# Optimization experiments

Measured on AMD Instinct MI355X. Metric: run time of the kernel, lower is better.

## Reference

```python
import jax, jax.numpy as jnp
import numpy as np

N = 100000      # nodes
E = 800000      # directed edges per branch
HID = 128
FOUT = 128
HEADS = 2
LAYERS = 3      # convlayer
JK_LAYERS = 3
H2 = (JK_LAYERS * HID) // 2   # PyG JK-LSTM hidden size = 192
N_AA = 26
N_SS = 3


def setup_inputs() -> dict:
    key = jax.random.key(0)
    ks = iter(jax.random.split(key, 32))
    def nrm(shape, scale=0.05):
        return jax.random.normal(next(ks), shape, dtype=jnp.float32) * scale
    return {
        "x_idx": jax.random.randint(next(ks), (N, 2), 0, N_SS),
        "x_flt": jax.random.normal(next(ks), (N, 5), dtype=jnp.float32),
        "edge_index_l": jax.random.randint(next(ks), (2, E), 0, N),
        "edge_index_r": jax.random.randint(next(ks), (2, E), 0, N),
        "emb_aa": nrm((2, N_AA, HID - 5)),          # [branch, vocab, hid-5]
        "emb_ss": nrm((2, N_SS, HID - 5)),
        "conv_W": nrm((2, LAYERS, HID, HEADS * HID)),
        "conv_att_src": nrm((2, LAYERS, HEADS, HID)),
        "conv_att_dst": nrm((2, LAYERS, HEADS, HID)),
        "conv_bias": nrm((2, LAYERS, HID)),
        "lstm_Wih": nrm((2, 2, 4 * H2, HID)),        # [branch, direction, 4H2, hid]
        "lstm_Whh": nrm((2, 2, 4 * H2, H2)),
        "lstm_bih": nrm((2, 2, 4 * H2)),
        "lstm_bhh": nrm((2, 2, 4 * H2)),
        "jk_att_W": nrm((2, 2 * H2)),
        "jk_att_b": nrm((2,)),
        "dummy_W": nrm((2, HID, HID)),
        "dummy_b": nrm((2, HID)),
        "fin_W": nrm((4, HID, FOUT)),
        "fin_b": nrm((4, FOUT)),
        "last_W": nrm((FOUT,)),                      # Linear(fout,1,bias=False)
    }


def _gat_conv(x, src, dst, W, att_src, att_dst, bias):
    # PyG GATConv, concat=False (mean over heads), leaky_relu slope 0.2
    n = x.shape[0]
    h, c = att_src.shape
    xh = (x @ W).reshape(n, h, c)                         # [N,H,C]
    a_src = jnp.einsum('nhc,hc->nh', xh, att_src)
    a_dst = jnp.einsum('nhc,hc->nh', xh, att_dst)
    e = jax.nn.leaky_relu(a_src[src] + a_dst[dst], 0.2)   # [E,H]
    m = jax.ops.segment_max(e, dst, num_segments=n)
    ex = jnp.exp(e - m[dst])
    denom = jax.ops.segment_sum(ex, dst, num_segments=n)
    alpha = ex / (denom[dst] + 1e-16)                     # segment softmax over dst
    out = jax.ops.segment_sum(xh[src] * alpha[:, :, None], dst, num_segments=n)
    return out.mean(axis=1) + bias                        # [N,C]


def _lstm_dir(xs, Wih, Whh, bih, bhh, reverse):
    # xs: [L,N,C]; single-layer LSTM, torch gate order i,f,g,o
    n = xs.shape[1]
    h2 = Whh.shape[1]
    b = bih + bhh
    def cell(carry, xt):
        h, c = carry
        g = xt @ Wih.T + h @ Whh.T + b
        i, f, gg, o = jnp.split(g, 4, axis=-1)
        c = jax.nn.sigmoid(f) * c + jax.nn.sigmoid(i) * jnp.tanh(gg)
        h = jax.nn.sigmoid(o) * jnp.tanh(c)
        return (h, c), h
    init = (jnp.zeros((n, h2), xs.dtype), jnp.zeros((n, h2), xs.dtype))
    _, hs = jax.lax.scan(cell, init, xs, reverse=reverse)
    return hs  # [L,N,H2]


def _jk(xs, Wih, Whh, bih, bhh, att_w, att_b):
    # PyG JumpingKnowledge('lstm'): bi-LSTM over layer axis + scalar attention
    hf = _lstm_dir(xs, Wih[0], Whh[0], bih[0], bhh[0], False)
    hb = _lstm_dir(xs, Wih[1], Whh[1], bih[1], bhh[1], True)
    h = jnp.concatenate([hf, hb], axis=-1)                # [L,N,2H2]
    a = jax.nn.softmax(jnp.einsum('lnh,h->ln', h, att_w) + att_b, axis=0)
    return (xs * a[..., None]).sum(axis=0)                # [N,C]


def _forward(x_idx, x_flt, edge_index_l, edge_index_r, emb_aa, emb_ss,
             conv_W, conv_att_src, conv_att_dst, conv_bias,
             lstm_Wih, lstm_Whh, lstm_bih, lstm_bhh, jk_att_W, jk_att_b,
             dummy_W, dummy_b, fin_W, fin_b, last_W):
    n = x_idx.shape[0]
    loops = jnp.arange(n)  # GATConv add_self_loops=True
    src_l = jnp.concatenate([edge_index_l[0], loops]); dst_l = jnp.concatenate([edge_index_l[1], loops])
    src_r = jnp.concatenate([edge_index_r[0], loops]); dst_r = jnp.concatenate([edge_index_r[1], loops])
    x_l = jnp.concatenate([emb_aa[0][x_idx[:, 0]] + emb_ss[0][x_idx[:, 1]], x_flt], axis=1)
    x_r = jnp.concatenate([emb_aa[1][x_idx[:, 0]] + emb_ss[1][x_idx[:, 1]], x_flt], axis=1)
    xs_l, xs_r = [], []
    for i in range(LAYERS):
        mean = (x_l + x_r) * 0.5
        o_l = mean + jax.nn.relu(_gat_conv(x_l, src_l, dst_l, conv_W[0, i], conv_att_src[0, i], conv_att_dst[0, i], conv_bias[0, i]))
        o_r = mean + jax.nn.relu(_gat_conv(x_r, src_r, dst_r, conv_W[1, i], conv_att_src[1, i], conv_att_dst[1, i], conv_bias[1, i]))
        x_l, x_r = o_l, o_r
        xs_l.append(x_l); xs_r.append(x_r)
    jk_l = _jk(jnp.stack(xs_l), lstm_Wih[0], lstm_Whh[0], lstm_bih[0], lstm_bhh[0], jk_att_W[0], jk_att_b[0])
    jk_r = _jk(jnp.stack(xs_r), lstm_Wih[1], lstm_Whh[1], lstm_bih[1], lstm_bhh[1], jk_att_W[1], jk_att_b[1])
    sq_l = jk_l @ dummy_W[0] + dummy_b[0]
    sq_r = jk_r @ dummy_W[1] + dummy_b[1]
    feats = [jk_l, sq_l, jk_r, sq_r]
    outs = [feats[i] @ fin_W[i] + fin_b[i] for i in range(4)]
    alpha = jax.nn.softmax(jnp.stack([o @ last_W for o in outs], axis=1), axis=1)  # [N,4]
    nodeemb = sum(outs[i] * alpha[:, i:i + 1] for i in range(4))
    return nodeemb


def reference(x_idx, x_flt, edge_index_l, edge_index_r, emb_aa, emb_ss,
              conv_W, conv_att_src, conv_att_dst, conv_bias,
              lstm_Wih, lstm_Whh, lstm_bih, lstm_bhh, jk_att_W, jk_att_b,
              dummy_W, dummy_b, fin_W, fin_b, last_W):
    return _forward(x_idx, x_flt, edge_index_l, edge_index_r, emb_aa, emb_ss,
                    conv_W, conv_att_src, conv_att_dst, conv_bias,
                    lstm_Wih, lstm_Whh, lstm_bih, lstm_bhh, jk_att_W, jk_att_b,
                    dummy_W, dummy_b, fin_W, fin_b, last_W)
```

## Files before the change

### kernel.cpp

```cpp
#include <hip/hip_runtime.h>
#include <cstddef>
#include <cstdint>

#define N_NODES 100000
#define N_EDGES 800000
#define EL_TOT  900000
#define HID 128
#define H2  192
#define G4  768
#define CH3 50000
#define BK  32
#define LDST 32
#define SCANB 98

typedef unsigned short bf16;
typedef __attribute__((ext_vector_type(8))) short bf16x8v;
typedef __attribute__((ext_vector_type(4))) float f32x4v;

#define AS1 __attribute__((address_space(1)))
#define AS3 __attribute__((address_space(3)))

__device__ __forceinline__ void async16(const bf16* g, bf16* l) {
    __builtin_amdgcn_global_load_lds((AS1 void*)g, (AS3 void*)l, 16, 0, 0);
}


__device__ __forceinline__ float b2f(bf16 u) {
    return __uint_as_float(((unsigned)u) << 16);
}
__device__ __forceinline__ bf16 f2b(float f) {
    unsigned u = __float_as_uint(f);
    u += 0x7FFFu + ((u >> 16) & 1u);
    return (bf16)(u >> 16);
}
__device__ __forceinline__ void stE(float* p, size_t i, float v) { p[i] = v; }
__device__ __forceinline__ void stE(bf16* p, size_t i, float v) { p[i] = f2b(v); }
__device__ __forceinline__ float ftanh(float x) {
    float cx = fminf(fmaxf(x, -15.f), 15.f);
    float e = __expf(2.f * cx);
    return (e - 1.f) / (e + 1.f);
}

__device__ __forceinline__ float x0_val(int c, int ia, int is_, int n,
                                        const float* __restrict__ embA,
                                        const float* __restrict__ embS,
                                        const float* __restrict__ xflt) {
    return (c < 123) ? (embA[ia * 123 + c] + embS[is_ * 123 + c])
                     : xflt[n * 5 + (c - 123)];
}

__device__ __forceinline__ int lstm_perm(int j) {
    int w = j & 63, tt = j >> 6;
    return (w >> 4) * 192 + tt * 16 + (w & 15);
}

__device__ __forceinline__ bool swz_tile(int R, int ntile, int& bm0, int& nt) {
    const int id = blockIdx.x;
    const int xcd = id & 7;
    const int s = id >> 3;
    nt = s % ntile;
    const int yp = (s / ntile) * 8 + xcd;
    if (yp * 128 >= R) return false;
    bm0 = yp * 128;
    return true;
}
static inline int swz_grid(int R, int ntile) {
    int panels = (R + 127) / 128;
    return 8 * ntile * ((panels + 7) / 8);
}


__global__ void sentinel_kernel(float* out, int n, float val) {
    int t = blockIdx.x * blockDim.x + threadIdx.x;
    if (t < n) out[t] = val;
}

__global__ void bsum_perm_kernel(const float* __restrict__ bih,
                                 const float* __restrict__ bhh,
                                 float* __restrict__ bsum) {
    int t = blockIdx.x * blockDim.x + threadIdx.x;
    if (t >= 4 * G4) return;
    int d = t / G4, j = t % G4;
    int orig = lstm_perm(j);
    bsum[t] = bih[d * G4 + orig] + bhh[d * G4 + orig];
}

__global__ void lstm_w_perm_kernel(const float* __restrict__ in,
                                   bf16* __restrict__ out, int K) {
    long long t = (long long)blockIdx.x * blockDim.x + threadIdx.x;
    long long tot = 4LL * G4 * K;
    if (t >= tot) return;
    int k = (int)(t % K);
    int j = (int)((t / K) % G4);
    int d = (int)(t / ((long long)G4 * K));
    int orig = lstm_perm(j);
    out[t] = f2b(in[((size_t)d * G4 + orig) * K + k]);
}

__global__ void trans_kernel(const float* __restrict__ in, bf16* __restrict__ out,
                             int batch, int K, int M) {
    long long t = (long long)blockIdx.x * blockDim.x + threadIdx.x;
    long long tot = (long long)batch * K * M;
    if (t >= tot) return;
    int per = K * M;
    int bt = (int)(t / per);
    int rem = (int)(t % per);
    int m = rem / K, k = rem % K;
    out[t] = f2b(in[(size_t)bt * per + (size_t)k * M + m]);
}


__global__ void deg_kernel(const int* __restrict__ dst, int* __restrict__ deg) {
    int t = blockIdx.x * blockDim.x + threadIdx.x;
    if (t >= EL_TOT) return;
    int d = (t < N_EDGES) ? dst[t] : (t - N_EDGES);
    atomicAdd(&deg[d], 1);
}

__global__ void scan1_kernel(const int* __restrict__ deg0, const int* __restrict__ deg1,
                             int* __restrict__ tmp0, int* __restrict__ tmp1,
                             int* __restrict__ bsums) {
    __shared__ int sdata[1024];
    const int b = blockIdx.y;
    const int* deg = b ? deg1 : deg0;
    int* tmp = b ? tmp1 : tmp0;
    int i = blockIdx.x * 1024 + threadIdx.x;
    int v = (i < N_NODES) ? deg[i] : 0;
    sdata[threadIdx.x] = v;
    __syncthreads();
    for (int off = 1; off < 1024; off <<= 1) {
        int t = (threadIdx.x >= (unsigned)off) ? sdata[threadIdx.x - off] : 0;
        __syncthreads();
        sdata[threadIdx.x] += t;
        __syncthreads();
    }
    if (i < N_NODES) tmp[i] = sdata[threadIdx.x];
    if (threadIdx.x == 1023) bsums[b * SCANB + blockIdx.x] = sdata[1023];
}

__global__ void scan2_kernel(int* __restrict__ bsums) {
    int b = threadIdx.x;
    if (b < 2) {
        int c = 0;
        for (int k = 0; k < SCANB; ++k) {
            int t = bsums[b * SCANB + k];
            bsums[b * SCANB + k] = c;
            c += t;
        }
    }
}

__global__ void scan3_kernel(const int* __restrict__ bsums,
                             const int* __restrict__ deg0, const int* __restrict__ deg1,
                             const int* __restrict__ tmp0, const int* __restrict__ tmp1,
                             int* __restrict__ offs0, int* __restrict__ offs1,
                             int* __restrict__ pos0, int* __restrict__ pos1) {
    const int b = blockIdx.y;
    const int* deg = b ? deg1 : deg0;
    const int* tmp = b ? tmp1 : tmp0;
    int* offs = b ? offs1 : offs0;
    int* pos = b ? pos1 : pos0;
    int carry = bsums[b * SCANB + blockIdx.x];
    int i = blockIdx.x * 1024 + threadIdx.x;
    if (i < N_NODES) {
        int inc = tmp[i] + carry;
        offs[i + 1] = inc;
        pos[i] = inc - deg[i];
    }
    if (i == 0) offs[0] = 0;
}

__global__ void fill_kernel(const int* __restrict__ srcrow,
                            const int* __restrict__ dstrow,
                            int* __restrict__ pos, int* __restrict__ srcs) {
    int t = blockIdx.x * blockDim.x + threadIdx.x;
    if (t >= EL_TOT) return;
    int s, d;
    if (t < N_EDGES) { s = srcrow[t]; d = dstrow[t]; }
    else             { s = d = t - N_EDGES; }
    int p = atomicAdd(&pos[d], 1);
    srcs[p] = s;
}

template<typename TC>
__device__ __forceinline__ void gemm128_body(
    const bf16* __restrict__ A1, const bf16* __restrict__ B1, int K1,
    const bf16* __restrict__ A2, const bf16* __restrict__ B2, int K2,
    TC* __restrict__ C, const float* __restrict__ bias, int R, int M,
    int bm0, int bn0) {
    __shared__ bf16 As[2][128 * LDST];
    __shared__ bf16 Bs[2][128 * LDST];
    const int tid = threadIdx.x;
    const int lane = tid & 63;
    const int wave = tid >> 6;
    const int wm = (wave & 1) * 64, wn = (wave >> 1) * 64;
    const int l15 = lane & 15;
    const int q8 = (lane >> 4) * 8;
    const int lr = lane >> 2;
    const int lc = (lane & 3) * 8;

    f32x4v acc[4][4];
#pragma unroll
    for (int i = 0; i < 4; ++i)
#pragma unroll
        for (int j = 0; j < 4; ++j) acc[i][j] = (f32x4v)(0.0f);

    const int n1 = K1 / BK;
    const int n2 = A2 ? (K2 / BK) : 0;
    const int ns = n1 + n2;

    auto stage = [&](int buf, int s) {
        const bf16* Ap; const bf16* Bp; int K, k0;
        if (s < n1) { Ap = A1; Bp = B1; K = K1; k0 = s * BK; }
        else        { Ap = A2; Bp = B2; K = K2; k0 = (s - n1) * BK; }
#pragma unroll
        for (int rnd = 0; rnd < 2; ++rnd) {
            const int rbase = wave * 16 + rnd * 64;
            const int row = rbase + lr;
            int ga = bm0 + row; ga = (ga < R) ? ga : (R - 1);
            async16(Ap + (size_t)ga * K + k0 + lc, &As[buf][rbase * LDST]);
            async16(Bp + (size_t)(bn0 + row) * K + k0 + lc, &Bs[buf][rbase * LDST]);
        }
    };

    stage(0, 0);
    __syncthreads();
    for (int s = 0; s < ns; ++s) {
        const int cur = s & 1;
        if (s + 1 < ns) stage(cur ^ 1, s + 1);
        bf16x8v af[4], bfv[4];
#pragma unroll
        for (int i = 0; i < 4; ++i) {
            af[i]  = *(const bf16x8v*)&As[cur][(wm + i * 16 + l15) * LDST + q8];
            bfv[i] = *(const bf16x8v*)&Bs[cur][(wn + i * 16 + l15) * LDST + q8];
        }
#pragma unroll
        for (int i = 0; i < 4; ++i)
#pragma unroll
            for (int j = 0; j < 4; ++j)
                acc[i][j] = __builtin_amdgcn_mfma_f32_16x16x32_bf16(
                    af[i], bfv[j], acc[i][j], 0, 0, 0);
        __syncthreads();
    }

#pragma unroll
    for (int i = 0; i < 4; ++i) {
        const int row0 = bm0 + wm + i * 16 + (lane >> 4) * 4;
#pragma unroll
        for (int j = 0; j < 4; ++j) {
            const int col = bn0 + wn + j * 16 + l15;
            const float bv = bias ? bias[col] : 0.f;
#pragma unroll
            for (int r = 0; r < 4; ++r) {
                const int gr = row0 + r;
                if (gr < R) stE(C, (size_t)gr * M + col, acc[i][j][r] + bv);
            }
        }
    }
}

template<typename TC>
__global__ __launch_bounds__(256) void mfma_gemm_kernel(
    const bf16* __restrict__ A1, const bf16* __restrict__ B1, int K1,
    const bf16* __restrict__ A2, const bf16* __restrict__ B2, int K2,
    TC* __restrict__ C, const float* __restrict__ bias, int R, int M) {
    int bm0, nt;
    if (!swz_tile(R, M >> 7, bm0, nt)) return;
    gemm128_body<TC>(A1, B1, K1, A2, B2, K2, C, bias, R, M, bm0, nt * 128);
}

template<typename TC>
__global__ __launch_bounds__(256) void mfma_gemm_b_kernel(
    const bf16* a0, const bf16* a1, const bf16* a2, const bf16* a3,
    const bf16* __restrict__ Bbase,
    TC* c0, TC* c1, TC* c2, TC* c3,
    const float* __restrict__ bias, int R) {
    int bm0, nt;
    if (!swz_tile(R, 1, bm0, nt)) return;
    const int y = blockIdx.y;
    const bf16* A1 = (y == 0) ? a0 : (y == 1) ? a1 : (y == 2) ? a2 : a3;
    TC* C = (y == 0) ? c0 : (y == 1) ? c1 : (y == 2) ? c2 : c3;
    gemm128_body<TC>(A1, Bbase + (size_t)y * 128 * 128, 128,
                     nullptr, nullptr, 0, C,
                     bias + (size_t)y * 128, R, 128, bm0, 0);
}

__global__ __launch_bounds__(256) void lstm_gemm2_kernel(
    const bf16* __restrict__ Ax0, const bf16* __restrict__ Ax1,
    const bf16* __restrict__ Wi, const bf16* __restrict__ Wh,
    const float* __restrict__ biasB,
    bf16* __restrict__ cS0, bf16* __restrict__ cS1,
    const bf16* __restrict__ hin0, const bf16* __restrict__ hin1,
    bf16* __restrict__ hout0, bf16* __restrict__ hout1,
    const float* __restrict__ awB,
    float* __restrict__ score0, float* __restrict__ score1,
    int first, int R) {
    __shared__ bf16 As[2][128 * LDST];
    __shared__ bf16 Bs[2][128 * LDST];
    int bm0, nt;
    if (!swz_tile(R, G4 >> 7, bm0, nt)) return;
    const int bn0 = nt * 128;
    const int y = blockIdx.y;
    const bf16* A1 = y ? Ax1 : Ax0;
    const bf16* B1 = Wi + (size_t)y * G4 * HID;
    const bf16* A2 = y ? hin1 : hin0;
    const bf16* B2 = Wh + (size_t)y * G4 * H2;
    const float* bias = biasB + (size_t)y * G4;
    bf16* c_state = y ? cS1 : cS0;
    bf16* h_out = y ? hout1 : hout0;
    const float* aw = awB + (size_t)y * H2;
    float* score = y ? score1 : score0;

    const int tid = threadIdx.x;
    const int lane = tid & 63;
    const int wave = tid >> 6;
    const int wm = (wave & 1) * 64, wn = (wave >> 1) * 64;
    const int l15 = lane & 15;
    const int q = lane >> 4;
    const int q8 = q * 8;
    const int lr = lane >> 2;
    const int lc = (lane & 3) * 8;

    f32x4v acc[4][4];
#pragma unroll
    for (int i = 0; i < 4; ++i)
#pragma unroll
        for (int j = 0; j < 4; ++j) acc[i][j] = (f32x4v)(0.0f);

    const int n1 = HID / BK;
    const int ns = n1 + (first ? 0 : (H2 / BK));

    auto stage = [&](int buf, int s) {
        const bf16* Ap; const bf16* Bp; int K, k0;
        if (s < n1) { Ap = A1; Bp = B1; K = HID; k0 = s * BK; }
        else        { Ap = A2; Bp = B2; K = H2;  k0 = (s - n1) * BK; }
#pragma unroll
        for (int rnd = 0; rnd < 2; ++rnd) {
            const int rbase = wave * 16 + rnd * 64;
            const int row = rbase + lr;
            int ga = bm0 + row; ga = (ga < R) ? ga : (R - 1);
            async16(Ap + (size_t)ga * K + k0 + lc, &As[buf][rbase * LDST]);
            async16(Bp + (size_t)(bn0 + row) * K + k0 + lc, &Bs[buf][rbase * LDST]);
        }
    };

    stage(0, 0);
    __syncthreads();
    for (int s = 0; s < ns; ++s) {
        const int cur = s & 1;
        if (s + 1 < ns) stage(cur ^ 1, s + 1);
        bf16x8v af[4], bfv[4];
#pragma unroll
        for (int i = 0; i < 4; ++i) {
            af[i]  = *(const bf16x8v*)&As[cur][(wm + i * 16 + l15) * LDST + q8];
            bfv[i] = *(const bf16x8v*)&Bs[cur][(wn + i * 16 + l15) * LDST + q8];
        }
#pragma unroll
        for (int i = 0; i < 4; ++i)
#pragma unroll
            for (int j = 0; j < 4; ++j)
                acc[i][j] = __builtin_amdgcn_mfma_f32_16x16x32_bf16(
                    af[i], bfv[j], acc[i][j], 0, 0, 0);
        __syncthreads();
    }

    const int u = ((bn0 + wn) >> 6) * 16 + l15;
    const float awu = aw[u];
    float bv[4];
#pragma unroll
    for (int j = 0; j < 4; ++j) bv[j] = bias[bn0 + wn + j * 16 + l15];
    float psum[4][4];
#pragma unroll
    for (int i = 0; i < 4; ++i) {
        const int row0 = bm0 + wm + i * 16 + q * 4;
#pragma unroll
        for (int r = 0; r < 4; ++r) {
            const int gr = row0 + r;
            const bool ok = gr < R;
            float ig = acc[i][0][r] + bv[0];
            float fg = acc[i][1][r] + bv[1];
            float gg = acc[i][2][r] + bv[2];
            float og = acc[i][3][r] + bv[3];
            float si = 1.f / (1.f + __expf(-ig));
            float sf = 1.f / (1.f + __expf(-fg));
            float so = 1.f / (1.f + __expf(-og));
            float co = (ok && !first) ? b2f(c_state[(size_t)gr * H2 + u]) : 0.f;
            float cn = sf * co + si * ftanh(gg);
            float hn = so * ftanh(cn);
            if (ok) {
                c_state[(size_t)gr * H2 + u] = f2b(cn);
                h_out[(size_t)gr * H2 + u] = f2b(hn);
            }
            psum[i][r] = hn * awu;
        }
    }
#pragma unroll
    for (int m = 1; m < 16; m <<= 1)
#pragma unroll
        for (int i = 0; i < 4; ++i)
#pragma unroll
            for (int r = 0; r < 4; ++r)
                psum[i][r] += __shfl_xor(psum[i][r], m);
    if (l15 == 0) {
#pragma unroll
        for (int i = 0; i < 4; ++i)
#pragma unroll
            for (int r = 0; r < 4; ++r) {
                const int gr = bm0 + wm + i * 16 + q * 4 + r;
                if (gr < R) atomicAdd(&score[gr], psum[i][r]);
            }
    }
}

__global__ __launch_bounds__(256) void mfma_gemm_x0_kernel(
    const int* __restrict__ xidx, const float* __restrict__ xflt,
    const float* __restrict__ embA, const float* __restrict__ embS,
    const bf16* __restrict__ B1, bf16* __restrict__ C, int R, int M) {
    __shared__ bf16 As[128 * LDST];
    __shared__ bf16 Bs[128 * LDST];
    int bm0, nt;
    if (!swz_tile(R, M >> 7, bm0, nt)) return;
    const int bn0 = nt * 128;
    const int tid = threadIdx.x;
    const int lane = tid & 63;
    const int wave = tid >> 6;
    const int wm = (wave & 1) * 64, wn = (wave >> 1) * 64;
    const int l15 = lane & 15;
    const int q8 = (lane >> 4) * 8;
    const int srow = tid >> 2;
    const int scol = (tid & 3) * 8;
    const int lr = lane >> 2;
    const int lc = (lane & 3) * 8;

    f32x4v acc[4][4];
#pragma unroll
    for (int i = 0; i < 4; ++i)
#pragma unroll
        for (int j = 0; j < 4; ++j) acc[i][j] = (f32x4v)(0.0f);

    for (int k0 = 0; k0 < 128; k0 += BK) {
#pragma unroll
        for (int rnd = 0; rnd < 2; ++rnd) {
            {
                int row = srow + rnd * 64;
                int ga = bm0 + row; ga = (ga < R) ? ga : (R - 1);
                int ia = xidx[2 * ga], is_ = xidx[2 * ga + 1];
                bf16 tmp[8];
#pragma unroll
                for (int t = 0; t < 8; ++t)
                    tmp[t] = f2b(x0_val(k0 + scol + t, ia, is_, ga, embA, embS, xflt));
                *(int4*)&As[row * LDST + scol] = *(const int4*)tmp;
            }
            {
                const int rbase = wave * 16 + rnd * 64;
                int row = rbase + lr;
                async16(B1 + (size_t)(bn0 + row) * 128 + k0 + lc, &Bs[rbase * LDST]);
            }
        }
        __syncthreads();
        bf16x8v af[4], bfv[4];
#pragma unroll
        for (int i = 0; i < 4; ++i) {
            af[i]  = *(const bf16x8v*)&As[(wm + i * 16 + l15) * LDST + q8];
            bfv[i] = *(const bf16x8v*)&Bs[(wn + i * 16 + l15) * LDST + q8];
        }
#pragma unroll
        for (int i = 0; i < 4; ++i)
#pragma unroll
            for (int j = 0; j < 4; ++j)
                acc[i][j] = __builtin_amdgcn_mfma_f32_16x16x32_bf16(
                    af[i], bfv[j], acc[i][j], 0, 0, 0);
        __syncthreads();
    }
#pragma unroll
    for (int i = 0; i < 4; ++i) {
        const int row0 = bm0 + wm + i * 16 + (lane >> 4) * 4;
#pragma unroll
        for (int j = 0; j < 4; ++j) {
            const int col = bn0 + wn + j * 16 + l15;
#pragma unroll
            for (int r = 0; r < 4; ++r) {
                const int gr = row0 + r;
                if (gr < R) C[(size_t)gr * M + col] = f2b(acc[i][j][r]);
            }
        }
    }
}


__device__ __forceinline__ float lrelu02(float x) { return x > 0.f ? x : 0.2f * x; }

__global__ __launch_bounds__(256) void agg_kernel(
    const bf16* __restrict__ xh, const float* __restrict__ as_,
    const float* __restrict__ ad_, const int* __restrict__ offs,
    const int* __restrict__ srcs,
    const bf16* __restrict__ xprev_l, const bf16* __restrict__ xprev_r,
    const int* __restrict__ xidx, const float* __restrict__ xflt,
    const float* __restrict__ embAl, const float* __restrict__ embSl,
    const float* __restrict__ embAr, const float* __restrict__ embSr,
    const float* __restrict__ bias, bf16* __restrict__ outx) {
    int n = (blockIdx.x * blockDim.x + threadIdx.x) >> 6;
    int lane = threadIdx.x & 63;
    if (n >= N_NODES) return;
    const int start = offs[n], end = offs[n + 1];
    const int l15 = lane & 15;
    const int g = lane >> 4;

    float av0[8], av1[8];
#pragma unroll
    for (int t = 0; t < 8; ++t) {
        av0[t] = as_[l15 * 8 + t];
        av1[t] = as_[128 + l15 * 8 + t];
    }

    float d0, d1;
    {
        uint2 v = *(const uint2*)(xh + (size_t)n * 256 + lane * 4);
        float p = ad_[lane * 4 + 0] * b2f((bf16)(v.x & 0xffffu))
                + ad_[lane * 4 + 1] * b2f((bf16)(v.x >> 16))
                + ad_[lane * 4 + 2] * b2f((bf16)(v.y & 0xffffu))
                + ad_[lane * 4 + 3] * b2f((bf16)(v.y >> 16));
        for (int o = 1; o < 32; o <<= 1) p += __shfl_xor(p, o);
        d0 = __shfl(p, 0);
        d1 = __shfl(p, 32);
    }

    float acc0[8] = {0, 0, 0, 0, 0, 0, 0, 0};
    float acc1[8] = {0, 0, 0, 0, 0, 0, 0, 0};
    float ds0 = 0.f, ds1 = 0.f;
#pragma unroll 2
    for (int j = start; j < end; j += 4) {
        int e = j + g;
        if (e < end) {
            int s = srcs[e];
            const bf16* row = xh + (size_t)s * 256 + l15 * 8;
            int4 v0 = *(const int4*)row;
            int4 v1 = *(const int4*)(row + 128);
            const int* w0 = (const int*)&v0;
            const int* w1 = (const int*)&v1;
            float x0[8], x1[8];
#pragma unroll
            for (int t = 0; t < 4; ++t) {
                x0[2 * t]     = __uint_as_float(((unsigned)w0[t]) << 16);
                x0[2 * t + 1] = __uint_as_float(((unsigned)w0[t]) & 0xffff0000u);
                x1[2 * t]     = __uint_as_float(((unsigned)w1[t]) << 16);
                x1[2 * t + 1] = __uint_as_float(((unsigned)w1[t]) & 0xffff0000u);
            }
            float p0 = 0.f, p1 = 0.f;
#pragma unroll
            for (int t = 0; t < 8; ++t) { p0 += av0[t] * x0[t]; p1 += av1[t] * x1[t]; }
#pragma unroll
            for (int m = 1; m < 16; m <<= 1) {
                p0 += __shfl_xor(p0, m);
                p1 += __shfl_xor(p1, m);
            }
            float al0 = __expf(lrelu02(p0 + d0));
            float al1 = __expf(lrelu02(p1 + d1));
            if (l15 == 0) { ds0 += al0; ds1 += al1; }
#pragma unroll
            for (int t = 0; t < 8; ++t) {
                acc0[t] += x0[t] * al0;
                acc1[t] += x1[t] * al1;
            }
        }
    }
#pragma unroll
    for (int t = 0; t < 8; ++t) {
        acc0[t] += __shfl_xor(acc0[t], 16); acc0[t] += __shfl_xor(acc0[t], 32);
        acc1[t] += __shfl_xor(acc1[t], 16); acc1[t] += __shfl_xor(acc1[t], 32);
    }
    ds0 += __shfl_xor(ds0, 16); ds0 += __shfl_xor(ds0, 32);
    ds1 += __shfl_xor(ds1, 16); ds1 += __shfl_xor(ds1, 32);
    ds0 = __shfl(ds0, 0); ds1 = __shfl(ds1, 0);
    const float inv0 = 1.f / (ds0 + 1e-16f);
    const float inv1 = 1.f / (ds1 + 1e-16f);
    float accm[8];
#pragma unroll
    for (int t = 0; t < 8; ++t)
        accm[t] = 0.5f * (acc0[t] * inv0 + acc1[t] * inv1);

    if (lane < 16) {
        const int c0 = l15 * 8;
        const size_t base = (size_t)n * HID + c0;
        float xm[8];
        if (xidx) {
            int ia = xidx[2 * n], is_ = xidx[2 * n + 1];
#pragma unroll
            for (int t = 0; t < 8; ++t)
                xm[t] = 0.5f * (x0_val(c0 + t, ia, is_, n, embAl, embSl, xflt) +
                                x0_val(c0 + t, ia, is_, n, embAr, embSr, xflt));
        } else {
            int4 vl = *(const int4*)(xprev_l + base);
            int4 vr = *(const int4*)(xprev_r + base);
            const int* wl = (const int*)&vl;
            const int* wr = (const int*)&vr;
#pragma unroll
            for (int t = 0; t < 4; ++t) {
                xm[2 * t] = 0.5f * (__uint_as_float(((unsigned)wl[t]) << 16) +
                                    __uint_as_float(((unsigned)wr[t]) << 16));
                xm[2 * t + 1] = 0.5f * (__uint_as_float(((unsigned)wl[t]) & 0xffff0000u) +
                                        __uint_as_float(((unsigned)wr[t]) & 0xffff0000u));
            }
        }
        bf16 res[8];
#pragma unroll
        for (int t = 0; t < 8; ++t)
            res[t] = f2b(xm[t] + fmaxf(0.f, accm[t] + bias[c0 + t]));
        *(int4*)(outx + base) = *(const int4*)res;
    }
}


__global__ __launch_bounds__(256) void jkfin_kernel(
    const float* __restrict__ sb, const bf16* __restrict__ xs0,
    const bf16* __restrict__ xs1, const bf16* __restrict__ xs2,
    bf16* __restrict__ jk) {
    int w = (blockIdx.x * blockDim.x + threadIdx.x) >> 6;
    int lane = threadIdx.x & 63;
    if (w >= N_NODES) return;
    float s0 = sb[w], s1 = sb[N_NODES + w], s2 = sb[2 * N_NODES + w];
    float m = fmaxf(s0, fmaxf(s1, s2));
    float a0 = __expf(s0 - m), a1 = __expf(s1 - m), a2 = __expf(s2 - m);
    float inv = 1.f / (a0 + a1 + a2);
    a0 *= inv; a1 *= inv; a2 *= inv;
    size_t gn = (size_t)w * HID + lane * 2;
#pragma unroll
    for (int t = 0; t < 2; ++t) {
        float v0 = b2f(xs0[gn + t]);
        float v1 = b2f(xs1[gn + t]);
        float v2 = b2f(xs2[gn + t]);
        jk[gn + t] = f2b(v0 * a0 + v1 * a1 + v2 * a2);
    }
}

__global__ __launch_bounds__(256) void final_kernel(
    const float* __restrict__ o0, const float* __restrict__ o1,
    const float* __restrict__ o2, const float* __restrict__ o3,
    const float* __restrict__ lw, float* __restrict__ out, int nloc, long long c3off) {
    int w = (blockIdx.x * blockDim.x + threadIdx.x) >> 6;
    int lane = threadIdx.x & 63;
    if (w >= nloc) return;
    size_t base = (size_t)w * HID;
    float w0 = lw[lane], w1 = lw[64 + lane];
    const float* op[4] = {o0, o1, o2, o3};
    float v[4][2];
    float s[4];
#pragma unroll
    for (int i = 0; i < 4; ++i) {
        v[i][0] = op[i][base + lane];
        v[i][1] = op[i][base + 64 + lane];
        float t = v[i][0] * w0 + v[i][1] * w1;
        for (int o = 1; o < 64; o <<= 1) t += __shfl_xor(t, o);
        s[i] = t;
    }
    float m = fmaxf(fmaxf(s[0], s[1]), fmaxf(s[2], s[3]));
    float e0 = __expf(s[0] - m), e1 = __expf(s[1] - m);
    float e2 = __expf(s[2] - m), e3 = __expf(s[3] - m);
    float inv = 1.f / (e0 + e1 + e2 + e3);
    float r0 = (v[0][0] * e0 + v[1][0] * e1 + v[2][0] * e2 + v[3][0] * e3) * inv;
    float r1 = (v[0][1] * e0 + v[1][1] * e1 + v[2][1] * e2 + v[3][1] * e3) * inv;
    size_t obase = (size_t)(c3off + w) * HID;
    out[obase + lane] = r0;
    out[obase + 64 + lane] = r1;
}


static long long align1k(long long x) { return (x + 1023) & ~1023LL; }

extern "C" void kernel_launch(void* const* d_in, const int* in_sizes, int n_in,
                              void* d_out, int out_size, void* d_ws, size_t ws_size,
                              hipStream_t stream) {
    (void)in_sizes; (void)n_in; (void)out_size;
    const int*   x_idx   = (const int*)  d_in[0];
    const float* x_flt   = (const float*)d_in[1];
    const int*   ei_l    = (const int*)  d_in[2];
    const int*   ei_r    = (const int*)  d_in[3];
    const float* emb_aa  = (const float*)d_in[4];
    const float* emb_ss  = (const float*)d_in[5];
    const float* conv_W  = (const float*)d_in[6];
    const float* att_s   = (const float*)d_in[7];
    const float* att_d   = (const float*)d_in[8];
    const float* conv_b  = (const float*)d_in[9];
    const float* Wih     = (const float*)d_in[10];
    const float* Whh     = (const float*)d_in[11];
    const float* bih     = (const float*)d_in[12];
    const float* bhh     = (const float*)d_in[13];
    const float* jkw     = (const float*)d_in[14];
    const float* dummy_W = (const float*)d_in[16];
    const float* dummy_b = (const float*)d_in[17];
    const float* fin_W   = (const float*)d_in[18];
    const float* fin_b   = (const float*)d_in[19];
    const float* last_W  = (const float*)d_in[20];
    float* out = (float*)d_out;

    const long long S = (long long)N_NODES * HID;
    char* ws = (char*)d_ws;
    long long off = 0;

    bf16* hist = (bf16*)(ws + off);  off += align1k(6 * S * 2);
    float* scores = (float*)(ws + off); off += align1k(6LL * N_NODES * 4);
    float* bsum   = (float*)(ws + off); off += align1k(4LL * G4 * 4);
    int* bsums    = (int*)(ws + off);  off += align1k(2LL * SCANB * 4);
    bf16* Wih_b   = (bf16*)(ws + off); off += align1k(4LL * G4 * HID * 2);
    bf16* Whh_b   = (bf16*)(ws + off); off += align1k(4LL * G4 * H2 * 2);
    bf16* dummyWt = (bf16*)(ws + off); off += align1k(2LL * 128 * 128 * 2);
    bf16* finWt   = (bf16*)(ws + off); off += align1k(4LL * 128 * 128 * 2);

    char* BIG = ws + off;
    const long long slot0 = align1k(2 * S * 2);
    const long long slot1 = align1k((long long)N_NODES * H2 * 2);
    const long long HS    = slot1;
    const long long need_seq = off + slot0 + slot1;
    const long long need_tB  = off + 5 * HS;

    if ((long long)ws_size < need_seq) {
        float val = 200000.0f + (float)(ws_size >> 20);
        sentinel_kernel<<<(N_NODES * HID + 255) / 256, 256, 0, stream>>>(
            out, N_NODES * HID, val);
        return;
    }
    const bool tierB = (long long)ws_size >= need_tB;

    bf16* xh  = (bf16*)BIG;
    bf16* jkb = (bf16*)BIG;
    int* ibase = (int*)(BIG + slot0);
    int *deg[2], *offs[2], *pos[2], *srcs[2];
    long long io = 0;
    for (int b = 0; b < 2; ++b) {
        deg[b]  = ibase + io; io += N_NODES;
        offs[b] = ibase + io; io += N_NODES + 1;
        pos[b]  = ibase + io; io += N_NODES;
        srcs[b] = ibase + io; io += EL_TOT;
    }
    long long io4a = ((io * 4 + 15) & ~15LL);
    bf16* convWt = (bf16*)(BIG + slot0 + io4a);
    bf16* hA = (bf16*)BIG;
    bf16* hB = (bf16*)d_out;
    bf16* cC = (bf16*)(BIG + slot0);
    bf16* cB0 = (bf16*)BIG;
    bf16* cB1 = (bf16*)(BIG + HS);
    bf16* hX0 = (bf16*)(BIG + 2 * HS);
    bf16* hX1 = (bf16*)(BIG + 3 * HS);
    bf16* hY0 = (bf16*)(BIG + 4 * HS);
    bf16* hY1 = (bf16*)d_out;

    const float* embA[2] = {emb_aa, emb_aa + 26 * 123};
    const float* embS[2] = {emb_ss, emb_ss + 3 * 123};

    bsum_perm_kernel<<<12, 256, 0, stream>>>(bih, bhh, bsum);
    trans_kernel<<<(6 * 128 * 256 + 255) / 256, 256, 0, stream>>>(
        conv_W, convWt, 6, 128, 256);
    lstm_w_perm_kernel<<<(4 * G4 * HID + 255) / 256, 256, 0, stream>>>(
        Wih, Wih_b, HID);
    lstm_w_perm_kernel<<<(4 * G4 * H2 + 255) / 256, 256, 0, stream>>>(
        Whh, Whh_b, H2);
    trans_kernel<<<(2 * 128 * 128 + 255) / 256, 256, 0, stream>>>(
        dummy_W, dummyWt, 2, 128, 128);
    trans_kernel<<<(4 * 128 * 128 + 255) / 256, 256, 0, stream>>>(
        fin_W, finWt, 4, 128, 128);
    hipMemsetAsync(deg[0], 0, N_NODES * sizeof(int), stream);
    hipMemsetAsync(deg[1], 0, N_NODES * sizeof(int), stream);
    deg_kernel<<<(EL_TOT + 255) / 256, 256, 0, stream>>>(ei_l + N_EDGES, deg[0]);
    deg_kernel<<<(EL_TOT + 255) / 256, 256, 0, stream>>>(ei_r + N_EDGES, deg[1]);
    scan1_kernel<<<dim3(SCANB, 2), 1024, 0, stream>>>(
        deg[0], deg[1], pos[0], pos[1], bsums);
    scan2_kernel<<<1, 64, 0, stream>>>(bsums);
    scan3_kernel<<<dim3(SCANB, 2), 1024, 0, stream>>>(
        bsums, deg[0], deg[1], pos[0], pos[1], offs[0], offs[1], pos[0], pos[1]);
    fill_kernel<<<(EL_TOT + 255) / 256, 256, 0, stream>>>(
        ei_l, ei_l + N_EDGES, pos[0], srcs[0]);
    fill_kernel<<<(EL_TOT + 255) / 256, 256, 0, stream>>>(
        ei_r, ei_r + N_EDGES, pos[1], srcs[1]);

    for (int i = 0; i < 3; ++i) {
        for (int b = 0; b < 2; ++b) {
            const bf16* Wc = convWt + (size_t)(b * 3 + i) * 256 * 128;
            if (i == 0) {
                mfma_gemm_x0_kernel<<<swz_grid(N_NODES, 2), 256, 0, stream>>>(
                    x_idx, x_flt, embA[b], embS[b], Wc, xh, N_NODES, 256);
            } else {
                mfma_gemm_kernel<bf16><<<swz_grid(N_NODES, 2), 256, 0, stream>>>(
                    hist + (size_t)(b * 3 + i - 1) * S, Wc, 128,
                    nullptr, nullptr, 0, xh, nullptr, N_NODES, 256);
            }
            const bf16* xpl = (i == 0) ? nullptr : hist + (size_t)(i - 1) * S;
            const bf16* xpr = (i == 0) ? nullptr : hist + (size_t)(3 + i - 1) * S;
            agg_kernel<<<25000, 256, 0, stream>>>(
                xh, att_s + (size_t)(b * 3 + i) * 2 * HID,
                att_d + (size_t)(b * 3 + i) * 2 * HID,
                offs[b], srcs[b], xpl, xpr,
                (i == 0) ? x_idx : nullptr, x_flt,
                embA[0], embS[0], embA[1], embS[1],
                conv_b + (size_t)(b * 3 + i) * HID, hist + (size_t)(b * 3 + i) * S);
        }
    }

    hipMemsetAsync(scores, 0, (size_t)6 * N_NODES * 4, stream);
    const int gx = swz_grid(N_NODES, 6);
    if (tierB) {
        for (int b = 0; b < 2; ++b) {
            const int c0 = b * 2;
            for (int st = 0; st < 3; ++st) {
                const int l0 = st, l1 = 2 - st;
                const bf16 *hin0, *hin1; bf16 *ho0, *ho1;
                if (st == 0)      { hin0 = hin1 = nullptr; ho0 = hX0; ho1 = hX1; }
                else if (st == 1) { hin0 = hX0; hin1 = hX1; ho0 = hY0; ho1 = hY1; }
                else              { hin0 = hY0; hin1 = hY1; ho0 = hX0; ho1 = hX1; }
                lstm_gemm2_kernel<<<dim3(gx, 2), 256, 0, stream>>>(
                    hist + (size_t)(b * 3 + l0) * S, hist + (size_t)(b * 3 + l1) * S,
                    Wih_b + (size_t)c0 * G4 * HID, Whh_b + (size_t)c0 * G4 * H2,
                    bsum + (size_t)c0 * G4,
                    cB0, cB1, hin0, hin1, ho0, ho1,
                    jkw + (size_t)b * 2 * H2,
                    scores + (size_t)(b * 3 + l0) * N_NODES,
                    scores + (size_t)(b * 3 + l1) * N_NODES,
                    st == 0 ? 1 : 0, N_NODES);
            }
        }
    } else {
        for (int b = 0; b < 2; ++b) {
            for (int dir = 0; dir < 2; ++dir) {
                const int combo = b * 2 + dir;
                for (int st = 0; st < 3; ++st) {
                    int l = dir ? (2 - st) : st;
                    const bf16* hin = (st == 0) ? nullptr : ((st & 1) ? hA : hB);
                    bf16* hout = (st & 1) ? hB : hA;
                    lstm_gemm2_kernel<<<dim3(gx, 1), 256, 0, stream>>>(
                        hist + (size_t)(b * 3 + l) * S, nullptr,
                        Wih_b + (size_t)combo * G4 * HID,
                        Whh_b + (size_t)combo * G4 * H2,
                        bsum + (size_t)combo * G4,
                        cC, nullptr, hin, nullptr, hout, nullptr,
                        jkw + (size_t)b * 2 * H2 + (size_t)dir * H2,
                        scores + (size_t)(b * 3 + l) * N_NODES, nullptr,
                        st == 0 ? 1 : 0, N_NODES);
                }
            }
        }
    }
    for (int b = 0; b < 2; ++b)
        jkfin_kernel<<<25000, 256, 0, stream>>>(
            scores + (size_t)b * 3 * N_NODES,
            hist + (size_t)b * 3 * S, hist + (size_t)(b * 3 + 1) * S,
            hist + (size_t)(b * 3 + 2) * S, jkb + (size_t)b * S);

    float* f3 = (float*)hist;
    bf16* jkl = jkb; bf16* jkr = jkb + S;
    for (long long c3 = 0; c3 < N_NODES; c3 += CH3) {
        int Rr = (int)((N_NODES - c3) < CH3 ? (N_NODES - c3) : CH3);
        float* o0 = f3;
        float* o1 = f3 + 1LL * CH3 * HID;
        float* o2 = f3 + 2LL * CH3 * HID;
        float* o3 = f3 + 3LL * CH3 * HID;
        bf16* sql = (bf16*)(f3 + 4LL * CH3 * HID);
        bf16* sqr = sql + (long long)CH3 * HID;
        mfma_gemm_b_kernel<bf16><<<dim3(swz_grid(Rr, 1), 2), 256, 0, stream>>>(
            jkl + c3 * HID, jkr + c3 * HID, nullptr, nullptr,
            dummyWt, sql, sqr, nullptr, nullptr, dummy_b, Rr);
        mfma_gemm_b_kernel<float><<<dim3(swz_grid(Rr, 1), 4), 256, 0, stream>>>(
            jkl + c3 * HID, sql, jkr + c3 * HID, sqr,
            finWt, o0, o1, o2, o3, fin_b, Rr);
        final_kernel<<<(Rr + 3) / 4, 256, 0, stream>>>(
            o0, o1, o2, o3, last_W, out, Rr, c3);
    }
}
```

Measured before the change: 2.998 ms.

## Widen GEMM tiles to 128x256 and precompute per-node source attention scores

Adds a 512-thread GEMM kernel with 128x256 tiles for the conv projection and widens the LSTM gate GEMM tiles the same way, so each block loads its A tile once for twice as many output columns. Adds a separate att_kernel that computes the per-node source attention logits once per layer. The aggregation kernel then reads two floats per edge instead of recomputing a 128-wide dot product and shuffle reduction for every edge. In exchange there is an extra kernel launch and a pass over xh, a scratch buffer for the logits, and a higher register load per block from the larger tiles.

Measured after the change: 3.277 ms. 1.09x slower.

```diff
diff --git a/kernel.cpp b/kernel.cpp
--- a/kernel.cpp
+++ b/kernel.cpp
@@ -185,7 +185,6 @@
 template<typename TC>
 __device__ __forceinline__ void gemm128_body(
     const bf16* __restrict__ A1, const bf16* __restrict__ B1, int K1,
-    const bf16* __restrict__ A2, const bf16* __restrict__ B2, int K2,
     TC* __restrict__ C, const float* __restrict__ bias, int R, int M,
     int bm0, int bn0) {
     __shared__ bf16 As[2][128 * LDST];
@@ -205,21 +204,16 @@
 #pragma unroll
         for (int j = 0; j < 4; ++j) acc[i][j] = (f32x4v)(0.0f);
 
-    const int n1 = K1 / BK;
-    const int n2 = A2 ? (K2 / BK) : 0;
-    const int ns = n1 + n2;
-
+    const int ns = K1 / BK;
     auto stage = [&](int buf, int s) {
-        const bf16* Ap; const bf16* Bp; int K, k0;
-        if (s < n1) { Ap = A1; Bp = B1; K = K1; k0 = s * BK; }
-        else        { Ap = A2; Bp = B2; K = K2; k0 = (s - n1) * BK; }
+        const int k0 = s * BK;
 #pragma unroll
         for (int rnd = 0; rnd < 2; ++rnd) {
             const int rbase = wave * 16 + rnd * 64;
             const int row = rbase + lr;
             int ga = bm0 + row; ga = (ga < R) ? ga : (R - 1);
-            async16(Ap + (size_t)ga * K + k0 + lc, &As[buf][rbase * LDST]);
-            async16(Bp + (size_t)(bn0 + row) * K + k0 + lc, &Bs[buf][rbase * LDST]);
+            async16(A1 + (size_t)ga * K1 + k0 + lc, &As[buf][rbase * LDST]);
+            async16(B1 + (size_t)(bn0 + row) * K1 + k0 + lc, &Bs[buf][rbase * LDST]);
         }
     };
 
@@ -257,16 +251,6 @@
             }
         }
     }
-}
-
-template<typename TC>
-__global__ __launch_bounds__(256) void mfma_gemm_kernel(
-    const bf16* __restrict__ A1, const bf16* __restrict__ B1, int K1,
-    const bf16* __restrict__ A2, const bf16* __restrict__ B2, int K2,
-    TC* __restrict__ C, const float* __restrict__ bias, int R, int M) {
-    int bm0, nt;
-    if (!swz_tile(R, M >> 7, bm0, nt)) return;
-    gemm128_body<TC>(A1, B1, K1, A2, B2, K2, C, bias, R, M, bm0, nt * 128);
 }
 
 template<typename TC>
@@ -280,12 +264,84 @@
     const int y = blockIdx.y;
     const bf16* A1 = (y == 0) ? a0 : (y == 1) ? a1 : (y == 2) ? a2 : a3;
     TC* C = (y == 0) ? c0 : (y == 1) ? c1 : (y == 2) ? c2 : c3;
-    gemm128_body<TC>(A1, Bbase + (size_t)y * 128 * 128, 128,
-                     nullptr, nullptr, 0, C,
+    gemm128_body<TC>(A1, Bbase + (size_t)y * 128 * 128, 128, C,
                      bias + (size_t)y * 128, R, 128, bm0, 0);
 }
 
-__global__ __launch_bounds__(256) void lstm_gemm2_kernel(
+__global__ __launch_bounds__(512) void mfma_gemm256_kernel(
+    const bf16* __restrict__ A1, const bf16* __restrict__ B1, int K1,
+    bf16* __restrict__ C, int R) {
+    __shared__ bf16 As[2][128 * LDST];
+    __shared__ bf16 Bs[2][256 * LDST];
+    int bm0, nt;
+    if (!swz_tile(R, 1, bm0, nt)) return;
+    const int tid = threadIdx.x;
+    const int lane = tid & 63;
+    const int wave = tid >> 6;
+    const int wm = (wave & 1) * 64;
+    const int wn = (wave >> 1) * 64;
+    const int l15 = lane & 15;
+    const int q8 = (lane >> 4) * 8;
+    const int lr = lane >> 2;
+    const int lc = (lane & 3) * 8;
+
+    f32x4v acc[4][4];
+#pragma unroll
+    for (int i = 0; i < 4; ++i)
+#pragma unroll
+        for (int j = 0; j < 4; ++j) acc[i][j] = (f32x4v)(0.0f);
+
+    const int ns = K1 / BK;
+    auto stage = [&](int buf, int s) {
+        const int k0 = s * BK;
+        {
+            const int rbase = wave * 16;
+            int ga = bm0 + rbase + lr; ga = (ga < R) ? ga : (R - 1);
+            async16(A1 + (size_t)ga * K1 + k0 + lc, &As[buf][rbase * LDST]);
+        }
+#pragma unroll
+        for (int rnd = 0; rnd < 2; ++rnd) {
+            const int rbase = rnd * 128 + wave * 16;
+            async16(B1 + (size_t)(rbase + lr) * K1 + k0 + lc, &Bs[buf][rbase * LDST]);
+        }
+    };
+
+    stage(0, 0);
+    __syncthreads();
+    for (int s = 0; s < ns; ++s) {
+        const int cur = s & 1;
+        if (s + 1 < ns) stage(cur ^ 1, s + 1);
+        bf16x8v af[4], bfv[4];
+#pragma unroll
+        for (int i = 0; i < 4; ++i) {
+            af[i]  = *(const bf16x8v*)&As[cur][(wm + i * 16 + l15) * LDST + q8];
+            bfv[i] = *(const bf16x8v*)&Bs[cur][(wn + i * 16 + l15) * LDST + q8];
+        }
+#pragma unroll
+        for (int i = 0; i < 4; ++i)
+#pragma unroll
+            for (int j = 0; j < 4; ++j)
+                acc[i][j] = __builtin_amdgcn_mfma_f32_16x16x32_bf16(
+                    af[i], bfv[j], acc[i][j], 0, 0, 0);
+        __syncthreads();
+    }
+
+#pragma unroll
+    for (int i = 0; i < 4; ++i) {
+        const int row0 = bm0 + wm + i * 16 + (lane >> 4) * 4;
+#pragma unroll
+        for (int j = 0; j < 4; ++j) {
+            const int col = wn + j * 16 + l15;
+#pragma unroll
+            for (int r = 0; r < 4; ++r) {
+                const int gr = row0 + r;
+                if (gr < R) C[(size_t)gr * 256 + col] = f2b(acc[i][j][r]);
+            }
+        }
+    }
+}
+
+__global__ __launch_bounds__(512) void lstm_gemm2_kernel(
     const bf16* __restrict__ Ax0, const bf16* __restrict__ Ax1,
     const bf16* __restrict__ Wi, const bf16* __restrict__ Wh,
     const float* __restrict__ biasB,
@@ -296,10 +352,10 @@
     float* __restrict__ score0, float* __restrict__ score1,
     int first, int R) {
     __shared__ bf16 As[2][128 * LDST];
-    __shared__ bf16 Bs[2][128 * LDST];
+    __shared__ bf16 Bs[2][256 * LDST];
     int bm0, nt;
-    if (!swz_tile(R, G4 >> 7, bm0, nt)) return;
-    const int bn0 = nt * 128;
+    if (!swz_tile(R, 3, bm0, nt)) return;
+    const int bn0 = nt * 256;
     const int y = blockIdx.y;
     const bf16* A1 = y ? Ax1 : Ax0;
     const bf16* B1 = Wi + (size_t)y * G4 * HID;
@@ -314,7 +370,8 @@
     const int tid = threadIdx.x;
     const int lane = tid & 63;
     const int wave = tid >> 6;
-    const int wm = (wave & 1) * 64, wn = (wave >> 1) * 64;
+    const int wm = (wave & 1) * 64;
+    const int wn = (wave >> 1) * 64;
     const int l15 = lane & 15;
     const int q = lane >> 4;
     const int q8 = q * 8;
@@ -334,13 +391,16 @@
         const bf16* Ap; const bf16* Bp; int K, k0;
         if (s < n1) { Ap = A1; Bp = B1; K = HID; k0 = s * BK; }
         else        { Ap = A2; Bp = B2; K = H2;  k0 = (s - n1) * BK; }
+        {
+            const int rbase = wave * 16;
+            int ga = bm0 + rbase + lr; ga = (ga < R) ? ga : (R - 1);
+            async16(Ap + (size_t)ga * K + k0 + lc, &As[buf][rbase * LDST]);
+        }
 #pragma unroll
         for (int rnd = 0; rnd < 2; ++rnd) {
-            const int rbase = wave * 16 + rnd * 64;
-            const int row = rbase + lr;
-            int ga = bm0 + row; ga = (ga < R) ? ga : (R - 1);
-            async16(Ap + (size_t)ga * K + k0 + lc, &As[buf][rbase * LDST]);
-            async16(Bp + (size_t)(bn0 + row) * K + k0 + lc, &Bs[buf][rbase * LDST]);
+            const int rbase = rnd * 128 + wave * 16;
+            async16(Bp + (size_t)(bn0 + rbase + lr) * K + k0 + lc,
+                    &Bs[buf][rbase * LDST]);
         }
     };
 
@@ -488,10 +548,29 @@
 }
 
 
+__global__ __launch_bounds__(256) void att_kernel(
+    const bf16* __restrict__ xh, const float* __restrict__ as_,
+    float* __restrict__ asrc) {
+    int w = (blockIdx.x * blockDim.x + threadIdx.x) >> 6;
+    int lane = threadIdx.x & 63;
+    if (w >= N_NODES) return;
+    const bf16* row = xh + (size_t)w * 256;
+    float x0 = b2f(row[lane]), x1 = b2f(row[64 + lane]);
+    float x2 = b2f(row[128 + lane]), x3 = b2f(row[192 + lane]);
+    float s0 = x0 * as_[lane] + x1 * as_[64 + lane];
+    float s1 = x2 * as_[128 + lane] + x3 * as_[192 + lane];
+    for (int o = 1; o < 64; o <<= 1) {
+        s0 += __shfl_xor(s0, o); s1 += __shfl_xor(s1, o);
+    }
+    if (lane == 0) {
+        asrc[2 * w] = s0; asrc[2 * w + 1] = s1;
+    }
+}
+
 __device__ __forceinline__ float lrelu02(float x) { return x > 0.f ? x : 0.2f * x; }
 
 __global__ __launch_bounds__(256) void agg_kernel(
-    const bf16* __restrict__ xh, const float* __restrict__ as_,
+    const bf16* __restrict__ xh, const float* __restrict__ asrc,
     const float* __restrict__ ad_, const int* __restrict__ offs,
     const int* __restrict__ srcs,
     const bf16* __restrict__ xprev_l, const bf16* __restrict__ xprev_r,
@@ -506,13 +585,6 @@
     const int l15 = lane & 15;
     const int g = lane >> 4;
 
-    float av0[8], av1[8];
-#pragma unroll
-    for (int t = 0; t < 8; ++t) {
-        av0[t] = as_[l15 * 8 + t];
-        av1[t] = as_[128 + l15 * 8 + t];
-    }
-
     float d0, d1;
     {
         uint2 v = *(const uint2*)(xh + (size_t)n * 256 + lane * 4);
@@ -533,34 +605,21 @@
         int e = j + g;
         if (e < end) {
             int s = srcs[e];
+            float2 a2 = *(const float2*)(asrc + 2 * s);
+            float al0 = __expf(lrelu02(a2.x + d0));
+            float al1 = __expf(lrelu02(a2.y + d1));
+            if (l15 == 0) { ds0 += al0; ds1 += al1; }
             const bf16* row = xh + (size_t)s * 256 + l15 * 8;
             int4 v0 = *(const int4*)row;
             int4 v1 = *(const int4*)(row + 128);
             const int* w0 = (const int*)&v0;
             const int* w1 = (const int*)&v1;
-            float x0[8], x1[8];
 #pragma unroll
             for (int t = 0; t < 4; ++t) {
-                x0[2 * t]     = __uint_as_float(((unsigned)w0[t]) << 16);
-                x0[2 * t + 1] = __uint_as_float(((unsigned)w0[t]) & 0xffff0000u);
-                x1[2 * t]     = __uint_as_float(((unsigned)w1[t]) << 16);
-                x1[2 * t + 1] = __uint_as_float(((unsigned)w1[t]) & 0xffff0000u);
-            }
-            float p0 = 0.f, p1 = 0.f;
-#pragma unroll
-            for (int t = 0; t < 8; ++t) { p0 += av0[t] * x0[t]; p1 += av1[t] * x1[t]; }
-#pragma unroll
-            for (int m = 1; m < 16; m <<= 1) {
-                p0 += __shfl_xor(p0, m);
-                p1 += __shfl_xor(p1, m);
-            }
-            float al0 = __expf(lrelu02(p0 + d0));
-            float al1 = __expf(lrelu02(p1 + d1));
-            if (l15 == 0) { ds0 += al0; ds1 += al1; }
-#pragma unroll
-            for (int t = 0; t < 8; ++t) {
-                acc0[t] += x0[t] * al0;
-                acc1[t] += x1[t] * al1;
+                acc0[2 * t]     += __uint_as_float(((unsigned)w0[t]) << 16) * al0;
+                acc0[2 * t + 1] += __uint_as_float(((unsigned)w0[t]) & 0xffff0000u) * al0;
+                acc1[2 * t]     += __uint_as_float(((unsigned)w1[t]) << 16) * al1;
+                acc1[2 * t + 1] += __uint_as_float(((unsigned)w1[t]) & 0xffff0000u) * al1;
             }
         }
     }
@@ -733,7 +792,8 @@
         srcs[b] = ibase + io; io += EL_TOT;
     }
     long long io4a = ((io * 4 + 15) & ~15LL);
-    bf16* convWt = (bf16*)(BIG + slot0 + io4a);
+    float* asrc = (float*)(BIG + slot0 + io4a);
+    bf16* convWt = (bf16*)(BIG + slot0 + io4a + 2LL * N_NODES * 4);
     bf16* hA = (bf16*)BIG;
     bf16* hB = (bf16*)d_out;
     bf16* cC = (bf16*)(BIG + slot0);
@@ -779,15 +839,15 @@
                 mfma_gemm_x0_kernel<<<swz_grid(N_NODES, 2), 256, 0, stream>>>(
                     x_idx, x_flt, embA[b], embS[b], Wc, xh, N_NODES, 256);
             } else {
-                mfma_gemm_kernel<bf16><<<swz_grid(N_NODES, 2), 256, 0, stream>>>(
-                    hist + (size_t)(b * 3 + i - 1) * S, Wc, 128,
-                    nullptr, nullptr, 0, xh, nullptr, N_NODES, 256);
-            }
+                mfma_gemm256_kernel<<<swz_grid(N_NODES, 1), 512, 0, stream>>>(
+                    hist + (size_t)(b * 3 + i - 1) * S, Wc, 128, xh, N_NODES);
+            }
+            att_kernel<<<25000, 256, 0, stream>>>(
+                xh, att_s + (size_t)(b * 3 + i) * 2 * HID, asrc);
             const bf16* xpl = (i == 0) ? nullptr : hist + (size_t)(i - 1) * S;
             const bf16* xpr = (i == 0) ? nullptr : hist + (size_t)(3 + i - 1) * S;
             agg_kernel<<<25000, 256, 0, stream>>>(
-                xh, att_s + (size_t)(b * 3 + i) * 2 * HID,
-                att_d + (size_t)(b * 3 + i) * 2 * HID,
+                xh, asrc, att_d + (size_t)(b * 3 + i) * 2 * HID,
                 offs[b], srcs[b], xpl, xpr,
                 (i == 0) ? x_idx : nullptr, x_flt,
                 embA[0], embS[0], embA[1], embS[1],
@@ -796,7 +856,7 @@
     }
 
     hipMemsetAsync(scores, 0, (size_t)6 * N_NODES * 4, stream);
-    const int gx = swz_grid(N_NODES, 6);
+    const int gx = swz_grid(N_NODES, 3);
     if (tierB) {
         for (int b = 0; b < 2; ++b) {
             const int c0 = b * 2;
@@ -806,7 +866,7 @@
                 if (st == 0)      { hin0 = hin1 = nullptr; ho0 = hX0; ho1 = hX1; }
                 else if (st == 1) { hin0 = hX0; hin1 = hX1; ho0 = hY0; ho1 = hY1; }
                 else              { hin0 = hY0; hin1 = hY1; ho0 = hX0; ho1 = hX1; }
-                lstm_gemm2_kernel<<<dim3(gx, 2), 256, 0, stream>>>(
+                lstm_gemm2_kernel<<<dim3(gx, 2), 512, 0, stream>>>(
                     hist + (size_t)(b * 3 + l0) * S, hist + (size_t)(b * 3 + l1) * S,
                     Wih_b + (size_t)c0 * G4 * HID, Whh_b + (size_t)c0 * G4 * H2,
                     bsum + (size_t)c0 * G4,
@@ -825,7 +885,7 @@
                     int l = dir ? (2 - st) : st;
                     const bf16* hin = (st == 0) ? nullptr : ((st & 1) ? hA : hB);
                     bf16* hout = (st & 1) ? hB : hA;
-                    lstm_gemm2_kernel<<<dim3(gx, 1), 256, 0, stream>>>(
+                    lstm_gemm2_kernel<<<dim3(gx, 1), 512, 0, stream>>>(
                         hist + (size_t)(b * 3 + l) * S, nullptr,
                         Wih_b + (size_t)combo * G4 * HID,
                         Whh_b + (size_t)combo * G4 * H2,
```
